# Performance work log

Hardware: AMD Instinct MI355X
Metric: run time of the kernel (lower is better)

## Reference

```python
import jax, jax.numpy as jnp
import numpy as np

# Config (matches init_kwargs + Mamba2 defaults: expand=2, headdim=64, ngroups=1)
B_, C_IN, T, H, W = 4, 23, 8, 128, 128
P = 4
DM = 256
D_STATE = 16
D_CONV = 4
EXPAND = 2
D_INNER = EXPAND * DM            # 512
HEADDIM = 64
NHEADS = D_INNER // HEADDIM      # 8
CONV_DIM = D_INNER + 2 * D_STATE # 544 (ngroups=1)
D_IN_PROJ = 2 * D_INNER + 2 * D_STATE + NHEADS


def setup_inputs() -> dict:
    key = jax.random.key(0)
    ks = jax.random.split(key, 12)
    s = lambda k, shape, sc: (jax.random.normal(k, shape, jnp.float32) * sc)
    x = jax.random.normal(ks[0], (B_, C_IN, T, H, W), jnp.float32)
    patch_w = s(ks[1], (DM, C_IN, P, P), 0.05)       # Conv3d weight, depth-1 dim squeezed
    patch_b = s(ks[2], (DM,), 0.02)
    W_in = s(ks[3], (DM, D_IN_PROJ), 0.05)           # in_proj (bias=False)
    conv_w = s(ks[4], (CONV_DIM, D_CONV), 0.2)       # depthwise conv1d weight
    conv_b = s(ks[5], (CONV_DIM,), 0.02)
    dt_bias = jnp.log(jnp.expm1(jnp.exp(jax.random.uniform(ks[6], (NHEADS,), jnp.float32, jnp.log(1e-3), jnp.log(1e-1)))))
    A_log = jnp.log(jnp.arange(1, NHEADS + 1, dtype=jnp.float32))
    D_param = jnp.ones((NHEADS,), jnp.float32)
    norm_w = jnp.ones((D_INNER,), jnp.float32)
    W_out = s(ks[7], (D_INNER, DM), 0.05)            # out_proj (bias=False)
    unembed_w = s(ks[8], (DM, C_IN, P, P), 0.05)     # ConvTranspose3d weight (in,out,1,p,p)
    unembed_b = s(ks[9], (C_IN,), 0.02)
    return {"x": x, "patch_w": patch_w, "patch_b": patch_b, "W_in": W_in,
            "conv_w": conv_w, "conv_b": conv_b, "dt_bias": dt_bias, "A_log": A_log,
            "D_param": D_param, "norm_w": norm_w, "W_out": W_out,
            "unembed_w": unembed_w, "unembed_b": unembed_b}


def reference(x, patch_w, patch_b, W_in, conv_w, conv_b, dt_bias, A_log,
              D_param, norm_w, W_out, unembed_w, unembed_b):
    B, C, Tt, Hh, Ww = x.shape
    p = patch_w.shape[-1]
    Hp, Wp = Hh // p, Ww // p
    L = Tt * Hp * Wp
    # --- Conv3d patch embed (kernel (1,p,p), stride (1,p,p)) == non-overlapping patchify ---
    xr = x.reshape(B, C, Tt, Hp, p, Wp, p)
    emb = jnp.einsum('bcthiwj,dcij->bthwd', xr, patch_w) + patch_b  # [B,T,Hp,Wp,D]
    xs = emb.reshape(B, L, DM)
    # --- Mamba2 ---
    zxbcdt = xs @ W_in                                 # [B,L,2*d_inner+2*d_state+nheads]
    z = zxbcdt[:, :, :D_INNER]
    xBC = zxbcdt[:, :, D_INNER:D_INNER + CONV_DIM]
    dt = zxbcdt[:, :, D_INNER + CONV_DIM:]             # [B,L,nheads]
    # causal depthwise conv1d + silu
    xp = jnp.pad(xBC, ((0, 0), (D_CONV - 1, 0), (0, 0)))
    conv_out = conv_b + sum(xp[:, k:k + L, :] * conv_w[:, k] for k in range(D_CONV))
    xBC = jax.nn.silu(conv_out)
    xh = xBC[:, :, :D_INNER].reshape(B, L, NHEADS, HEADDIM)
    Bm = xBC[:, :, D_INNER:D_INNER + D_STATE]          # [B,L,N] (ngroups=1)
    Cm = xBC[:, :, D_INNER + D_STATE:]                 # [B,L,N]
    dt = jax.nn.softplus(dt + dt_bias)                 # [B,L,H]
    A = -jnp.exp(A_log)                                # [H]
    dA = jnp.exp(dt * A)                               # [B,L,H]
    xdt = xh * dt[..., None]                           # [B,L,H,P]
    # selective state-space scan: h_t = dA_t h_{t-1} + (dt_t x_t) B_t^T ; y_t = h_t C_t
    def step(h, inp):
        dA_t, xdt_t, B_t, C_t = inp
        h = dA_t[..., None, None] * h + jnp.einsum('bhp,bn->bhpn', xdt_t, B_t)
        y = jnp.einsum('bhpn,bn->bhp', h, C_t)
        return h, y
    inps = (dA.transpose(1, 0, 2), xdt.transpose(1, 0, 2, 3),
            Bm.transpose(1, 0, 2), Cm.transpose(1, 0, 2))
    h0 = jnp.zeros((B, NHEADS, HEADDIM, D_STATE), xs.dtype)
    _, ys = jax.lax.scan(step, h0, inps)               # [L,B,H,P]
    y = ys.transpose(1, 0, 2, 3) + D_param[None, None, :, None] * xh
    y = y.reshape(B, L, D_INNER)
    # gated RMSNorm (norm_before_gate=False): rmsnorm(y * silu(z)) * w
    yg = y * jax.nn.silu(z)
    y = yg * jax.lax.rsqrt(jnp.mean(yg * yg, axis=-1, keepdims=True) + 1e-5) * norm_w
    out_seq = y @ W_out                                # [B,L,DM]
    # --- ConvTranspose3d unembed (kernel (1,p,p), stride (1,p,p)) == un-patchify ---
    outp = out_seq.reshape(B, Tt, Hp, Wp, DM)
    un = jnp.einsum('bthwd,dcij->bcthiwj', outp, unembed_w)
    out = un.reshape(B, C, Tt, Hh, Ww) + unembed_b[None, :, None, None, None]
    return out + x
```

## Files before the change

### kernel.cpp

```cpp
#include <hip/hip_runtime.h>
#include <hip/hip_bf16.h>
#include <cstdint>
#include <cstddef>

#define B_N       4
#define C_INCH    23
#define T_N       8
#define W_IMG     128
#define L_SEQ     8192
#define BLROWS    32768
#define DM_       256
#define D_INNER_  512
#define CONV_DIM_ 544
#define D_PROJ    1064
#define KPATCH    368
#define QCH       64
#define NCH       128
#define RECW      48
#define PFD       8

typedef unsigned short ushort_t;
typedef unsigned int uint_t;
typedef __attribute__((ext_vector_type(8))) short short8;
typedef __attribute__((ext_vector_type(4))) float f32x4;

__device__ __forceinline__ float b2f(ushort_t u) {
    union { float f; uint_t u; } v; v.u = ((uint_t)u) << 16; return v.f;
}
__device__ __forceinline__ ushort_t f2b(float f) {
    union { float f; uint_t u; } v; v.f = f;
    uint_t r = v.u + 0x7fffu + ((v.u >> 16) & 1u);
    return (ushort_t)(r >> 16);
}

__device__ __forceinline__ void gload_lds16(const ushort_t* g, ushort_t* l) {
    __builtin_amdgcn_global_load_lds(
        (const __attribute__((address_space(1))) unsigned int*)g,
        (__attribute__((address_space(3))) unsigned int*)l, 16, 0, 0);
}

__global__ void k_transcast(const float* __restrict__ src, ushort_t* __restrict__ dst,
                            int K, int N, const float* __restrict__ rscale) {
    int n = blockIdx.x;
    for (int k = threadIdx.x; k < K; k += 256) {
        float v = 0.f;
        if (n < N) {
            v = src[(size_t)k * N + n];
            if (rscale) v *= rscale[k];
        }
        dst[(size_t)n * K + k] = f2b(v);
    }
}

__global__ void k_castpad(const float* __restrict__ src, ushort_t* __restrict__ dst) {
    int d = blockIdx.x; int k = threadIdx.x;
    dst[d * 384 + k] = (k < KPATCH) ? f2b(src[d * KPATCH + k]) : (ushort_t)0;
}

__global__ void __launch_bounds__(256) k_pgemm(const float* __restrict__ x,
                                               const ushort_t* __restrict__ Wt,
                                               ushort_t* __restrict__ Cv,
                                               const float* __restrict__ bias) {
    __shared__ ushort_t Al[128 * 64];
    __shared__ ushort_t Bl[128 * 64];
    const int tid = threadIdx.x;
    const int w = tid >> 6, lane = tid & 63;
    const int wr = w >> 1, wc = w & 1;
    const int rowbase = blockIdx.y * 128;
    const int colbase = blockIdx.x * 128;
    const int g = lane >> 4, r = lane & 15;
    const int b  = rowbase >> 13;
    const int t  = (rowbase >> 10) & 7;
    const int hp0 = (rowbase >> 5) & 31;

    f32x4 acc[4][4];
    #pragma unroll
    for (int i = 0; i < 4; ++i)
        #pragma unroll
        for (int j = 0; j < 4; ++j) acc[i][j] = (f32x4){0.f, 0.f, 0.f, 0.f};

    for (int it = 0; it < 6; ++it) {
        int k0 = it * 64;
        __syncthreads();
        #pragma unroll
        for (int i2 = 0; i2 < 4; ++i2) {
            int s = i2 * 256 + (w << 6) + lane;
            int row = s >> 3;
            int c16 = (s & 7) ^ (row & 7);
            gload_lds16(Wt + (size_t)(colbase + row) * 384 + k0 + c16 * 8,
                        &Bl[(size_t)(i2 * 256 + (w << 6)) * 8]);
        }
        #pragma unroll
        for (int i2 = 0; i2 < 8; ++i2) {
            int idx = i2 * 256 + tid;
            int row = idx >> 4, kq = idx & 15;
            int c = (k0 >> 4) + (kq >> 2);
            int i = kq & 3;
            uint_t u0 = 0, u1 = 0;
            if (c < C_INCH) {
                int hp = hp0 + (row >> 5), wp = row & 31;
                const float4 v = *(const float4*)&x[(((size_t)(b * C_INCH + c) * T_N + t) << 14)
                                                    + (size_t)(hp * 4 + i) * W_IMG + wp * 4];
                u0 = (uint_t)f2b(v.x) | ((uint_t)f2b(v.y) << 16);
                u1 = (uint_t)f2b(v.z) | ((uint_t)f2b(v.w) << 16);
            }
            int slot = (row << 3) + ((kq >> 1) ^ (row & 7));
            *(uint2*)&Al[(size_t)slot * 8 + (kq & 1) * 4] = make_uint2(u0, u1);
        }
        __syncthreads();

        short8 af[2][4], bf[2][4];
        #pragma unroll
        for (int ks = 0; ks < 2; ++ks)
            #pragma unroll
            for (int mi = 0; mi < 4; ++mi) {
                int row = (wr << 6) + (mi << 4) + r;
                int c16 = ((ks << 2) | g) ^ (row & 7);
                af[ks][mi] = *(const short8*)&Al[(size_t)((row << 3) + c16) * 8];
            }
        #pragma unroll
        for (int ks = 0; ks < 2; ++ks)
            #pragma unroll
            for (int ni = 0; ni < 4; ++ni) {
                int row = (wc << 6) + (ni << 4) + r;
                int c16 = ((ks << 2) | g) ^ (row & 7);
                bf[ks][ni] = *(const short8*)&Bl[(size_t)((row << 3) + c16) * 8];
            }
        #pragma unroll
        for (int ks = 0; ks < 2; ++ks)
            #pragma unroll
            for (int mi = 0; mi < 4; ++mi)
                #pragma unroll
                for (int ni = 0; ni < 4; ++ni)
                    acc[mi][ni] = __builtin_amdgcn_mfma_f32_16x16x32_bf16(
                        af[ks][mi], bf[ks][ni], acc[mi][ni], 0, 0, 0);
    }

    #pragma unroll
    for (int mi = 0; mi < 4; ++mi) {
        int rw = rowbase + (wr << 6) + (mi << 4) + (g << 2);
        #pragma unroll
        for (int ni = 0; ni < 4; ++ni) {
            int col = colbase + (wc << 6) + (ni << 4) + r;
            float bv = bias[col];
            f32x4 v = acc[mi][ni];
            #pragma unroll
            for (int j = 0; j < 4; ++j)
                Cv[(size_t)(rw + j) * DM_ + col] = f2b(v[j] + bv);
        }
    }
}

template <int K, int N, bool CBF, bool ASCALE>
__global__ void __launch_bounds__(256) k_mgemm(const ushort_t* __restrict__ A, const int lda,
                                               const ushort_t* __restrict__ Wt,
                                               void* __restrict__ Cv, const int ldc, const int coff,
                                               const float* __restrict__ bias) {
    __shared__ ushort_t Al[128 * 64];
    __shared__ ushort_t Bl[128 * 64];
    const int tid = threadIdx.x;
    const int w = tid >> 6, lane = tid & 63;
    const int wr = w >> 1, wc = w & 1;
    const int rowbase = blockIdx.y * 128;
    const int colbase = blockIdx.x * 128;
    const int g = lane >> 4, r = lane & 15;

    f32x4 acc[4][4];
    #pragma unroll
    for (int i = 0; i < 4; ++i)
        #pragma unroll
        for (int j = 0; j < 4; ++j) acc[i][j] = (f32x4){0.f, 0.f, 0.f, 0.f};
    float rs[4] = {0.f, 0.f, 0.f, 0.f};

    for (int k0 = 0; k0 < K; k0 += 64) {
        __syncthreads();
        #pragma unroll
        for (int it = 0; it < 4; ++it) {
            int s = it * 256 + (w << 6) + lane;
            int row = s >> 3;
            int c16 = (s & 7) ^ (row & 7);
            gload_lds16(A + (size_t)(rowbase + row) * lda + k0 + c16 * 8,
                        &Al[(size_t)(it * 256 + (w << 6)) * 8]);
        }
        #pragma unroll
        for (int it = 0; it < 4; ++it) {
            int s = it * 256 + (w << 6) + lane;
            int row = s >> 3;
            int c16 = (s & 7) ^ (row & 7);
            gload_lds16(Wt + (size_t)(colbase + row) * K + k0 + c16 * 8,
                        &Bl[(size_t)(it * 256 + (w << 6)) * 8]);
        }
        __syncthreads();

        short8 af[2][4], bf[2][4];
        #pragma unroll
        for (int ks = 0; ks < 2; ++ks)
            #pragma unroll
            for (int mi = 0; mi < 4; ++mi) {
                int row = (wr << 6) + (mi << 4) + r;
                int c16 = ((ks << 2) | g) ^ (row & 7);
                af[ks][mi] = *(const short8*)&Al[(size_t)((row << 3) + c16) * 8];
            }
        #pragma unroll
        for (int ks = 0; ks < 2; ++ks)
            #pragma unroll
            for (int ni = 0; ni < 4; ++ni) {
                int row = (wc << 6) + (ni << 4) + r;
                int c16 = ((ks << 2) | g) ^ (row & 7);
                bf[ks][ni] = *(const short8*)&Bl[(size_t)((row << 3) + c16) * 8];
            }
        if (ASCALE) {
            #pragma unroll
            for (int ks = 0; ks < 2; ++ks)
                #pragma unroll
                for (int mi = 0; mi < 4; ++mi)
                    #pragma unroll
                    for (int e = 0; e < 8; ++e) {
                        float v = b2f((ushort_t)af[ks][mi][e]);
                        rs[mi] += v * v;
                    }
        }
        #pragma unroll
        for (int ks = 0; ks < 2; ++ks)
            #pragma unroll
            for (int mi = 0; mi < 4; ++mi)
                #pragma unroll
                for (int ni = 0; ni < 4; ++ni)
                    acc[mi][ni] = __builtin_amdgcn_mfma_f32_16x16x32_bf16(
                        af[ks][mi], bf[ks][ni], acc[mi][ni], 0, 0, 0);
    }

    #pragma unroll
    for (int mi = 0; mi < 4; ++mi) {
        int rw = rowbase + (wr << 6) + (mi << 4) + (g << 2);
        float sj[4] = {1.f, 1.f, 1.f, 1.f};
        if (ASCALE) {
            float s = rs[mi];
            s += __shfl_xor(s, 16);
            s += __shfl_xor(s, 32);
            float sc = rsqrtf(s * (1.f / 512.f) + 1e-5f);
            #pragma unroll
            for (int j = 0; j < 4; ++j) sj[j] = __shfl(sc, 4 * g + j);
        }
        #pragma unroll
        for (int ni = 0; ni < 4; ++ni) {
            int col = colbase + (wc << 6) + (ni << 4) + r;
            if (col < N) {
                float bv = bias ? bias[col] : 0.f;
                f32x4 v = acc[mi][ni];
                #pragma unroll
                for (int j = 0; j < 4; ++j) {
                    size_t cidx = (size_t)(rw + j) * ldc + coff + col;
                    float vr = v[j] * sj[j] + bv;
                    if (CBF) ((ushort_t*)Cv)[cidx] = f2b(vr);
                    else     ((float*)Cv)[cidx]   = vr;
                }
            }
        }
    }
}

__global__ void __launch_bounds__(256) k_conv(const ushort_t* __restrict__ xbcdt,
                                              const float* __restrict__ cw,
                                              const float* __restrict__ cb,
                                              const float* __restrict__ dtb,
                                              const float* __restrict__ alog,
                                              ushort_t* __restrict__ xbc,
                                              float* __restrict__ brec) {
    int tid = threadIdx.x;
    int rb = blockIdx.x * 8;
    int srb = rb & (L_SEQ - 1);
    #pragma unroll
    for (int it = 0; it < 3; ++it) {
        int ch = it * 256 + tid;
        if (ch >= 552) break;
        if (ch < CONV_DIM_) {
            float w0 = cw[ch * 4 + 0], w1 = cw[ch * 4 + 1];
            float w2 = cw[ch * 4 + 2], w3 = cw[ch * 4 + 3];
            float bias = cb[ch];
            float win[11];
            #pragma unroll
            for (int j = 0; j < 11; ++j) {
                int sj = srb + j - 3;
                win[j] = (sj >= 0) ? b2f(xbcdt[(size_t)(rb + j - 3) * 640 + ch]) : 0.f;
            }
            #pragma unroll
            for (int r = 0; r < 8; ++r) {
                float acc = bias + win[r] * w0 + win[r + 1] * w1 + win[r + 2] * w2 + win[r + 3] * w3;
                float s = acc / (1.f + __expf(-acc));
                size_t row = rb + r;
                if (ch < 512) xbc[row * 512 + ch] = f2b(s);
                else          brec[row * RECW + (ch - 512)] = s;
            }
        } else {
            int h = ch - CONV_DIM_;
            float A = -__expf(alog[h]);
            float db = dtb[h];
            #pragma unroll
            for (int r = 0; r < 8; ++r) {
                size_t row = rb + r;
                float v = b2f(xbcdt[row * 640 + ch]) + db;
                float sp = (v > 20.f) ? v : log1pf(__expf(v));
                brec[row * RECW + 32 + h] = __expf(sp * A);
                brec[row * RECW + 40 + h] = sp;
            }
        }
    }
}

__global__ void __launch_bounds__(256) k_scan1(const ushort_t* __restrict__ xbc,
                                               const float* __restrict__ brec,
                                               float* __restrict__ sbuf,
                                               float* __restrict__ cdf) {
    __shared__ float rec[QCH * RECW];
    int c = blockIdx.x, b = blockIdx.z;
    int tid = threadIdx.x;
    int h = blockIdx.y * 4 + (tid >> 6);
    int p = tid & 63;
    int off = h * 64 + p;
    size_t row0 = (size_t)b * L_SEQ + (size_t)c * QCH;

    {
        const float4* src = (const float4*)(brec + row0 * RECW);
        float4* dst = (float4*)rec;
        #pragma unroll
        for (int i = 0; i < 3; ++i) dst[i * 256 + tid] = src[i * 256 + tid];
    }

    float st[16];
    #pragma unroll
    for (int n = 0; n < 16; ++n) st[n] = 0.f;
    float cd = 1.f;
    float xh[PFD];
    #pragma unroll
    for (int j = 0; j < PFD; ++j) xh[j] = b2f(xbc[(row0 + j) * 512 + off]);
    __syncthreads();

    for (int s0 = 0; s0 < QCH; s0 += PFD) {
        float xhn[PFD];
        #pragma unroll
        for (int j = 0; j < PFD; ++j)
            xhn[j] = b2f(xbc[(row0 + s0 + PFD + j) * 512 + off]);
        #pragma unroll
        for (int j = 0; j < PFD; ++j) {
            const float* r = rec + (s0 + j) * RECW;
            float da  = r[32 + h];
            float dtt = r[40 + h];
            float xdt = xh[j] * dtt;
            const float4* B4 = (const float4*)r;
            #pragma unroll
            for (int q = 0; q < 4; ++q) {
                float4 Bv = B4[q];
                st[q*4+0] = da * st[q*4+0] + xdt * Bv.x;
                st[q*4+1] = da * st[q*4+1] + xdt * Bv.y;
                st[q*4+2] = da * st[q*4+2] + xdt * Bv.z;
                st[q*4+3] = da * st[q*4+3] + xdt * Bv.w;
            }
            cd *= da;
        }
        #pragma unroll
        for (int j = 0; j < PFD; ++j) xh[j] = xhn[j];
    }
    size_t base = (size_t)((b * 8 + h) * NCH + c) * 1024 + p * 16;
    #pragma unroll
    for (int q = 0; q < 4; ++q)
        *(float4*)&sbuf[base + q * 4] = make_float4(st[q*4], st[q*4+1], st[q*4+2], st[q*4+3]);
    if (p == 0) cdf[(b * 8 + h) * NCH + c] = cd;
}

__global__ void __launch_bounds__(256) k_chain(const float* __restrict__ sbuf,
                                               const float* __restrict__ cdf,
                                               float* __restrict__ hin) {
    int h = blockIdx.x, b = blockIdx.y;
    int tid = threadIdx.x;
    float4 H = make_float4(0.f, 0.f, 0.f, 0.f);
    size_t base = (size_t)((b * 8 + h) * NCH) * 1024;
    for (int c = 0; c < NCH; ++c) {
        *(float4*)&hin[base + (size_t)c * 1024 + tid * 4] = H;
        float cdfv = cdf[(b * 8 + h) * NCH + c];
        float4 S = *(const float4*)&sbuf[base + (size_t)c * 1024 + tid * 4];
        H.x = cdfv * H.x + S.x;
        H.y = cdfv * H.y + S.y;
        H.z = cdfv * H.z + S.z;
        H.w = cdfv * H.w + S.w;
    }
}

__global__ void __launch_bounds__(512) k_scan2(const ushort_t* __restrict__ xbc,
                                               const ushort_t* __restrict__ z_bf,
                                               const float* __restrict__ brec,
                                               const float* __restrict__ Dp,
                                               const float* __restrict__ hin,
                                               ushort_t* __restrict__ yg_out) {
    __shared__ float rec[QCH * RECW];
    int c = blockIdx.x, b = blockIdx.y;
    int tid = threadIdx.x;
    int h = tid >> 6, p = tid & 63;
    int off = h * 64 + p;
    size_t row0 = (size_t)b * L_SEQ + (size_t)c * QCH;

    {
        const float4* src = (const float4*)(brec + row0 * RECW);
        float4* dst = (float4*)rec;
        dst[tid] = src[tid];
        if (tid < 256) dst[512 + tid] = src[512 + tid];
    }

    float st[16];
    const float4* H = (const float4*)&hin[(size_t)((b * 8 + h) * NCH + c) * 1024 + p * 16];
    #pragma unroll
    for (int q = 0; q < 4; ++q) {
        float4 Hv = H[q];
        st[q*4+0] = Hv.x; st[q*4+1] = Hv.y; st[q*4+2] = Hv.z; st[q*4+3] = Hv.w;
    }
    float Dh = Dp[h];
    float xh[PFD], zz[PFD];
    #pragma unroll
    for (int j = 0; j < PFD; ++j) {
        xh[j] = b2f(xbc[(row0 + j) * 512 + off]);
        zz[j] = b2f(z_bf[(row0 + j) * 512 + off]);
    }
    __syncthreads();

    for (int s0 = 0; s0 < QCH; s0 += PFD) {
        float xhn[PFD], zzn[PFD];
        #pragma unroll
        for (int j = 0; j < PFD; ++j) {
            size_t rn = row0 + s0 + PFD + j;
            xhn[j] = b2f(xbc[rn * 512 + off]);
            zzn[j] = b2f(z_bf[rn * 512 + off]);
        }
        #pragma unroll
        for (int j = 0; j < PFD; ++j) {
            const float* r = rec + (s0 + j) * RECW;
            float da  = r[32 + h];
            float dtt = r[40 + h];
            float xdt = xh[j] * dtt;
            const float4* B4 = (const float4*)r;
            const float4* C4 = (const float4*)(r + 16);
            float d0 = 0.f, d1 = 0.f, d2 = 0.f, d3 = 0.f;
            #pragma unroll
            for (int q = 0; q < 4; ++q) {
                float4 Bv = B4[q];
                float4 Cv = C4[q];
                st[q*4+0] = da * st[q*4+0] + xdt * Bv.x;
                st[q*4+1] = da * st[q*4+1] + xdt * Bv.y;
                st[q*4+2] = da * st[q*4+2] + xdt * Bv.z;
                st[q*4+3] = da * st[q*4+3] + xdt * Bv.w;
                d0 += st[q*4+0] * Cv.x;
                d1 += st[q*4+1] * Cv.y;
                d2 += st[q*4+2] * Cv.z;
                d3 += st[q*4+3] * Cv.w;
            }
            float y = (d0 + d1) + (d2 + d3) + Dh * xh[j];
            float ygv = y * (zz[j] / (1.f + __expf(-zz[j])));
            yg_out[(row0 + s0 + j) * 512 + off] = f2b(ygv);
        }
        #pragma unroll
        for (int j = 0; j < PFD; ++j) { xh[j] = xhn[j]; zz[j] = zzn[j]; }
    }
}

__global__ void __launch_bounds__(256) k_scatter(const ushort_t* __restrict__ tmp,
                                                 const float* __restrict__ ub,
                                                 const float* __restrict__ xin,
                                                 float* __restrict__ out) {
    int tid = threadIdx.x;
    int w = tid & 127;
    int h = (blockIdx.x << 1) | (tid >> 7);
    int c = blockIdx.y >> 3, t = blockIdx.y & 7;
    int b = blockIdx.z;
    size_t row = (size_t)b * L_SEQ + t * 1024 + (h >> 2) * 32 + (w >> 2);
    int kk = c * 16 + (h & 3) * 4 + (w & 3);
    size_t oidx = (((size_t)(b * C_INCH + c) * T_N + t) << 14) + (size_t)h * W_IMG + w;
    out[oidx] = b2f(tmp[row * KPATCH + kk]) + ub[c] + xin[oidx];
}

extern "C" void kernel_launch(void* const* d_in, const int* in_sizes, int n_in,
                              void* d_out, int out_size, void* d_ws, size_t ws_size,
                              hipStream_t stream) {
    const float* x       = (const float*)d_in[0];
    const float* patch_w = (const float*)d_in[1];
    const float* patch_b = (const float*)d_in[2];
    const float* W_in    = (const float*)d_in[3];
    const float* conv_w  = (const float*)d_in[4];
    const float* conv_b  = (const float*)d_in[5];
    const float* dt_bias = (const float*)d_in[6];
    const float* A_log   = (const float*)d_in[7];
    const float* D_param = (const float*)d_in[8];
    const float* norm_w  = (const float*)d_in[9];
    const float* W_out   = (const float*)d_in[10];
    const float* unemb_w = (const float*)d_in[11];
    const float* unemb_b = (const float*)d_in[12];
    float* out = (float*)d_out;

    char* p = (char*)d_ws;
    ushort_t* scratch = (ushort_t*)p; p += (size_t)BLROWS * 384 * 2;
    float* cdf  = (float*)p;   p += (size_t)32 * NCH * 4;
    float* sbuf = (float*)p;   p += (size_t)32 * NCH * 1024 * 4;
    float* hin  = (float*)p;   p += (size_t)32 * NCH * 1024 * 4;
    float* brec = (float*)p;   p += (size_t)BLROWS * RECW * 4;
    ushort_t* Wt_p   = (ushort_t*)p; p += (size_t)256 * 384 * 2;
    ushort_t* Wt_in  = (ushort_t*)p; p += (size_t)1152 * 256 * 2;
    ushort_t* Wt_out = (ushort_t*)p; p += (size_t)256 * 512 * 2;
    ushort_t* Wt_un  = (ushort_t*)p; p += (size_t)384 * 256 * 2;
    ushort_t* xs     = (ushort_t*)p; p += (size_t)BLROWS * DM_ * 2;
    ushort_t* xbc    = (ushort_t*)p; p += (size_t)BLROWS * 512 * 2;
    ushort_t* z_bf   = (ushort_t*)p; p += (size_t)BLROWS * 512 * 2;
    ushort_t* xbcdt  = (ushort_t*)p; p += (size_t)BLROWS * 640 * 2;
    size_t need = (size_t)(p - (char*)d_ws);
    if (ws_size < need) return;

    ushort_t* tmp = scratch;
    ushort_t* yg  = xbcdt;

    k_castpad<<<256, 384, 0, stream>>>(patch_w, Wt_p);
    k_transcast<<<1152, 256, 0, stream>>>(W_in, Wt_in, 256, 1064, nullptr);
    k_transcast<<<256, 256, 0, stream>>>(W_out, Wt_out, 512, 256, norm_w);
    k_transcast<<<384, 256, 0, stream>>>(unemb_w, Wt_un, 256, 368, nullptr);

    k_pgemm<<<dim3(2, 256), 256, 0, stream>>>(x, Wt_p, xs, patch_b);

    k_mgemm<256, 512, true, false><<<dim3(4, 256), 256, 0, stream>>>(xs, 256, Wt_in, z_bf, 512, 0, nullptr);
    k_mgemm<256, 552, true, false><<<dim3(5, 256), 256, 0, stream>>>(xs, 256, Wt_in + (size_t)512 * 256, xbcdt, 640, 0, nullptr);

    k_conv<<<BLROWS / 8, 256, 0, stream>>>(xbcdt, conv_w, conv_b, dt_bias, A_log, xbc, brec);

    k_scan1<<<dim3(NCH, 2, 4), 256, 0, stream>>>(xbc, brec, sbuf, cdf);
    k_chain<<<dim3(8, 4), 256, 0, stream>>>(sbuf, cdf, hin);
    k_scan2<<<dim3(NCH, 4), 512, 0, stream>>>(xbc, z_bf, brec, D_param, hin, yg);

    k_mgemm<512, 256, true, true><<<dim3(2, 256), 256, 0, stream>>>(yg, 512, Wt_out, xs, DM_, 0, nullptr);

    k_mgemm<256, 368, true, false><<<dim3(3, 256), 256, 0, stream>>>(xs, 256, Wt_un, tmp, KPATCH, 0, nullptr);

    k_scatter<<<dim3(64, 184, 4), 256, 0, stream>>>(tmp, unemb_b, x, out);
}
```

Before: 259.6 us.

## Replace sequential intra-chunk scan with SSD-style MFMA chunked matmul

```diff
diff --git a/kernel.cpp b/kernel.cpp
--- a/kernel.cpp
+++ b/kernel.cpp
@@ -16,7 +16,7 @@
 #define KPATCH    368
 #define QCH       64
 #define NCH       128
-#define RECW      48
+#define RECW      56
 #define PFD       8
 
 typedef unsigned short ushort_t;
@@ -37,6 +37,21 @@
     __builtin_amdgcn_global_load_lds(
         (const __attribute__((address_space(1))) unsigned int*)g,
         (__attribute__((address_space(3))) unsigned int*)l, 16, 0, 0);
+}
+
+__device__ __forceinline__ short8 frag8(const float* q, bool live) {
+    short8 f;
+    if (live) {
+        float4 lo = *(const float4*)q, hi = *(const float4*)(q + 4);
+        f[0] = (short)f2b(lo.x); f[1] = (short)f2b(lo.y);
+        f[2] = (short)f2b(lo.z); f[3] = (short)f2b(lo.w);
+        f[4] = (short)f2b(hi.x); f[5] = (short)f2b(hi.y);
+        f[6] = (short)f2b(hi.z); f[7] = (short)f2b(hi.w);
+    } else {
+        #pragma unroll
+        for (int e = 0; e < 8; ++e) f[e] = 0;
+    }
+    return f;
 }
 
 __global__ void k_transcast(const float* __restrict__ src, ushort_t* __restrict__ dst,
@@ -303,6 +318,7 @@
                 float sp = (v > 20.f) ? v : log1pf(__expf(v));
                 brec[row * RECW + 32 + h] = __expf(sp * A);
                 brec[row * RECW + 40 + h] = sp;
+                brec[row * RECW + 48 + h] = sp * A;
             }
         }
     }
@@ -325,6 +341,7 @@
         float4* dst = (float4*)rec;
         #pragma unroll
         for (int i = 0; i < 3; ++i) dst[i * 256 + tid] = src[i * 256 + tid];
+        if (tid < 128) dst[768 + tid] = src[768 + tid];
     }
 
     float st[16];
@@ -386,78 +403,117 @@
     }
 }
 
-__global__ void __launch_bounds__(512) k_scan2(const ushort_t* __restrict__ xbc,
-                                               const ushort_t* __restrict__ z_bf,
-                                               const float* __restrict__ brec,
-                                               const float* __restrict__ Dp,
-                                               const float* __restrict__ hin,
-                                               ushort_t* __restrict__ yg_out) {
-    __shared__ float rec[QCH * RECW];
-    int c = blockIdx.x, b = blockIdx.y;
-    int tid = threadIdx.x;
-    int h = tid >> 6, p = tid & 63;
-    int off = h * 64 + p;
-    size_t row0 = (size_t)b * L_SEQ + (size_t)c * QCH;
-
+__global__ void __launch_bounds__(64) k_ssc2(const ushort_t* __restrict__ xbc,
+                                             const ushort_t* __restrict__ z_bf,
+                                             const float* __restrict__ brec,
+                                             const float* __restrict__ Dp,
+                                             const float* __restrict__ hin,
+                                             ushort_t* __restrict__ yg_out) {
+    __shared__ ushort_t XhT[64 * 72];
+    __shared__ ushort_t Pl [64 * 72];
+    __shared__ float Sl[64], Tl[64], El[64];
+    const int c = blockIdx.x, h = blockIdx.y, b = blockIdx.z;
+    const int lane = threadIdx.x;
+    const int g = lane >> 4, r = lane & 15;
+    const size_t row0 = (size_t)b * L_SEQ + (size_t)c * QCH;
+    const size_t bhc = (size_t)(b * 8 + h) * NCH + c;
+
+    uint4 xw[8];
     {
-        const float4* src = (const float4*)(brec + row0 * RECW);
-        float4* dst = (float4*)rec;
-        dst[tid] = src[tid];
-        if (tid < 256) dst[512 + tid] = src[512 + tid];
-    }
-
-    float st[16];
-    const float4* H = (const float4*)&hin[(size_t)((b * 8 + h) * NCH + c) * 1024 + p * 16];
-    #pragma unroll
-    for (int q = 0; q < 4; ++q) {
-        float4 Hv = H[q];
-        st[q*4+0] = Hv.x; st[q*4+1] = Hv.y; st[q*4+2] = Hv.z; st[q*4+3] = Hv.w;
-    }
-    float Dh = Dp[h];
-    float xh[PFD], zz[PFD];
-    #pragma unroll
-    for (int j = 0; j < PFD; ++j) {
-        xh[j] = b2f(xbc[(row0 + j) * 512 + off]);
-        zz[j] = b2f(z_bf[(row0 + j) * 512 + off]);
+        const uint4* xsrc = (const uint4*)(xbc + (row0 + lane) * 512 + h * 64);
+        #pragma unroll
+        for (int q = 0; q < 8; ++q) xw[q] = xsrc[q];
+    }
+    float ldA = brec[(row0 + lane) * RECW + 48 + h];
+    float dtv = brec[(row0 + lane) * RECW + 40 + h];
+
+    float S = ldA;
+    #pragma unroll
+    for (int d = 1; d < 64; d <<= 1) {
+        float o = __shfl(S, (lane >= d) ? (lane - d) : 0);
+        if (lane >= d) S += o;
+    }
+    Sl[lane] = S;
+    Tl[lane] = S - __logf(dtv);
+    El[lane] = __expf(S);
+
+    #pragma unroll
+    for (int p = 0; p < 64; ++p) {
+        uint4 v = xw[p >> 3];
+        int sub = (p >> 1) & 3;
+        uint_t word = (sub == 0) ? v.x : (sub == 1) ? v.y : (sub == 2) ? v.z : v.w;
+        XhT[p * 72 + lane] = (ushort_t)((p & 1) ? (word >> 16) : (word & 0xffffu));
+    }
+
+    short8 cwf[4], bwf[4];
+    #pragma unroll
+    for (int t4 = 0; t4 < 4; ++t4) {
+        cwf[t4] = frag8(brec + (row0 + t4 * 16 + r) * RECW + 16 + g * 8, g < 2);
+        bwf[t4] = frag8(brec + (row0 + t4 * 16 + r) * RECW + 0  + g * 8, g < 2);
     }
     __syncthreads();
 
-    for (int s0 = 0; s0 < QCH; s0 += PFD) {
-        float xhn[PFD], zzn[PFD];
-        #pragma unroll
-        for (int j = 0; j < PFD; ++j) {
-            size_t rn = row0 + s0 + PFD + j;
-            xhn[j] = b2f(xbc[rn * 512 + off]);
-            zzn[j] = b2f(z_bf[rn * 512 + off]);
-        }
-        #pragma unroll
-        for (int j = 0; j < PFD; ++j) {
-            const float* r = rec + (s0 + j) * RECW;
-            float da  = r[32 + h];
-            float dtt = r[40 + h];
-            float xdt = xh[j] * dtt;
-            const float4* B4 = (const float4*)r;
-            const float4* C4 = (const float4*)(r + 16);
-            float d0 = 0.f, d1 = 0.f, d2 = 0.f, d3 = 0.f;
-            #pragma unroll
-            for (int q = 0; q < 4; ++q) {
-                float4 Bv = B4[q];
-                float4 Cv = C4[q];
-                st[q*4+0] = da * st[q*4+0] + xdt * Bv.x;
-                st[q*4+1] = da * st[q*4+1] + xdt * Bv.y;
-                st[q*4+2] = da * st[q*4+2] + xdt * Bv.z;
-                st[q*4+3] = da * st[q*4+3] + xdt * Bv.w;
-                d0 += st[q*4+0] * Cv.x;
-                d1 += st[q*4+1] * Cv.y;
-                d2 += st[q*4+2] * Cv.z;
-                d3 += st[q*4+3] * Cv.w;
-            }
-            float y = (d0 + d1) + (d2 + d3) + Dh * xh[j];
-            float ygv = y * (zz[j] / (1.f + __expf(-zz[j])));
-            yg_out[(row0 + s0 + j) * 512 + off] = f2b(ygv);
-        }
-        #pragma unroll
-        for (int j = 0; j < PFD; ++j) { xh[j] = xhn[j]; zz[j] = zzn[j]; }
+    #pragma unroll
+    for (int j0t = 0; j0t < 4; ++j0t) {
+        #pragma unroll
+        for (int i0t = 0; i0t < 4; ++i0t) {
+            f32x4 m = (f32x4){0.f, 0.f, 0.f, 0.f};
+            m = __builtin_amdgcn_mfma_f32_16x16x32_bf16(bwf[j0t], cwf[i0t], m, 0, 0, 0);
+            int i = i0t * 16 + r;
+            float si = Sl[i];
+            float4 tj = *(const float4*)&Tl[j0t * 16 + g * 4];
+            ushort_t pv[4];
+            #pragma unroll
+            for (int reg = 0; reg < 4; ++reg) {
+                int j = j0t * 16 + g * 4 + reg;
+                float tjv = (reg == 0) ? tj.x : (reg == 1) ? tj.y : (reg == 2) ? tj.z : tj.w;
+                float mask = (j <= i) ? __expf(si - tjv) : 0.f;
+                pv[reg] = f2b(m[reg] * mask);
+            }
+            uint2 packed = make_uint2((uint_t)pv[0] | ((uint_t)pv[1] << 16),
+                                      (uint_t)pv[2] | ((uint_t)pv[3] << 16));
+            *(uint2*)&Pl[i * 72 + j0t * 16 + g * 4] = packed;
+        }
+    }
+    __syncthreads();
+
+    short8 xhf[4][2];
+    #pragma unroll
+    for (int p0t = 0; p0t < 4; ++p0t)
+        #pragma unroll
+        for (int kk = 0; kk < 2; ++kk)
+            xhf[p0t][kk] = *(const short8*)&XhT[(p0t * 16 + r) * 72 + kk * 32 + g * 8];
+    short8 hinf[4];
+    #pragma unroll
+    for (int p0t = 0; p0t < 4; ++p0t)
+        hinf[p0t] = frag8(hin + bhc * 1024 + (size_t)(p0t * 16 + r) * 16 + g * 8, g < 2);
+
+    const float Dh = Dp[h];
+
+    #pragma unroll
+    for (int i0t = 0; i0t < 4; ++i0t) {
+        short8 pa0 = *(const short8*)&Pl[(i0t * 16 + r) * 72 + 0  + g * 8];
+        short8 pa1 = *(const short8*)&Pl[(i0t * 16 + r) * 72 + 32 + g * 8];
+        float4 e4 = *(const float4*)&El[i0t * 16 + g * 4];
+        #pragma unroll
+        for (int p0t = 0; p0t < 4; ++p0t) {
+            f32x4 acc = (f32x4){0.f, 0.f, 0.f, 0.f};
+            acc = __builtin_amdgcn_mfma_f32_16x16x32_bf16(cwf[i0t], hinf[p0t], acc, 0, 0, 0);
+            acc[0] *= e4.x; acc[1] *= e4.y; acc[2] *= e4.z; acc[3] *= e4.w;
+            acc = __builtin_amdgcn_mfma_f32_16x16x32_bf16(pa0, xhf[p0t][0], acc, 0, 0, 0);
+            acc = __builtin_amdgcn_mfma_f32_16x16x32_bf16(pa1, xhf[p0t][1], acc, 0, 0, 0);
+            int p = p0t * 16 + r;
+            #pragma unroll
+            for (int reg = 0; reg < 4; ++reg) {
+                int i = i0t * 16 + g * 4 + reg;
+                size_t row = row0 + i;
+                float xhv = b2f(XhT[p * 72 + i]);
+                float y = acc[reg] + Dh * xhv;
+                float zz = b2f(z_bf[row * 512 + h * 64 + p]);
+                float ygv = y * (zz / (1.f + __expf(-zz)));
+                yg_out[row * 512 + h * 64 + p] = f2b(ygv);
+            }
+        }
     }
 }
 
@@ -528,7 +584,7 @@
 
     k_scan1<<<dim3(NCH, 2, 4), 256, 0, stream>>>(xbc, brec, sbuf, cdf);
     k_chain<<<dim3(8, 4), 256, 0, stream>>>(sbuf, cdf, hin);
-    k_scan2<<<dim3(NCH, 4), 512, 0, stream>>>(xbc, z_bf, brec, D_param, hin, yg);
+    k_ssc2<<<dim3(NCH, 8, 4), 64, 0, stream>>>(xbc, z_bf, brec, D_param, hin, yg);
 
     k_mgemm<512, 256, true, true><<<dim3(2, 256), 256, 0, stream>>>(yg, 512, Wt_out, xs, DM_, 0, nullptr);
 
```

Result: no change. 256.6 us (-1.2%).
